# Performance work log

Hardware: AMD Instinct MI355X
Metric: run time of the kernel (lower is better)

The kernel has to match this reference:

```python
import jax, jax.numpy as jnp
import numpy as np

N, B, DIN = 128, 2, 128
D, DFF, NHEAD, NLAYERS = 256, 1024, 8, 2
BLOCK = 32
LENGTH = 160


def setup_inputs() -> dict:
    key = jax.random.key(0)
    ks = jax.random.split(key, 10)
    r = lambda k, sh: jax.random.normal(k, sh, jnp.float32) * 0.05
    return {
        "inputs": jax.random.normal(ks[0], (N, B, DIN), jnp.float32),
        "in_W1": r(ks[1], (DIN, DFF)), "in_b1": jnp.zeros((DFF,), jnp.float32),
        "in_W2": r(ks[2], (DFF, D)), "in_b2": jnp.zeros((D,), jnp.float32),
        "k_W1": r(ks[3], (DIN, DFF)), "k_b1": jnp.zeros((DFF,), jnp.float32),
        "k_W2": r(ks[4], (DFF, 2)), "k_b2": jnp.zeros((2,), jnp.float32),
        "Wqkv": r(ks[5], (NLAYERS, D, 3 * D)), "bqkv": jnp.zeros((NLAYERS, 3 * D), jnp.float32),
        "Wo": r(ks[6], (NLAYERS, D, D)), "bo": jnp.zeros((NLAYERS, D), jnp.float32),
        "ln1_g": jnp.ones((NLAYERS, D), jnp.float32), "ln1_b": jnp.zeros((NLAYERS, D), jnp.float32),
        "W1": r(ks[7], (NLAYERS, D, DFF)), "b1": jnp.zeros((NLAYERS, DFF), jnp.float32),
        "W2": r(ks[8], (NLAYERS, DFF, D)), "b2": jnp.zeros((NLAYERS, D), jnp.float32),
        "ln2_g": jnp.ones((NLAYERS, D), jnp.float32), "ln2_b": jnp.zeros((NLAYERS, D), jnp.float32),
        "length": LENGTH,
    }


def _ln(x, g, b):
    m = jnp.mean(x, axis=-1, keepdims=True)
    v = jnp.mean(jnp.square(x - m), axis=-1, keepdims=True)
    return (x - m) * jax.lax.rsqrt(v + 1e-5) * g + b


def _forward(inputs, in_W1, in_b1, in_W2, in_b2, k_W1, k_b1, k_W2, k_b2,
             Wqkv, bqkv, Wo, bo, ln1_g, ln1_b, W1, b1, W2, b2, ln2_g, ln2_b, length):
    n, b, din = inputs.shape
    d = in_W2.shape[1]
    H, dh = NHEAD, in_W2.shape[1] // NHEAD
    Wmax = 2 * BLOCK + 1
    L = length
    idx = jnp.arange(n)
    starts = jnp.maximum(0, idx - BLOCK)                 # [N]
    ends = jnp.minimum(L, idx + BLOCK + 1)               # [N]
    cols = starts[:, None] + jnp.arange(Wmax)[None, :]   # [N,Wmax] absolute column per window slot
    valid = cols < ends[:, None]                          # [N,Wmax] ragged-window mask

    # sinusoidal PE at absolute column positions (start_idx = max(0, i-block))
    pos = cols.astype(jnp.float32)
    div = jnp.exp(jnp.arange(0, din, 2, dtype=jnp.float32) * (-np.log(10000.0) / din))
    ang = pos[..., None] * div                            # [N,Wmax,din/2]
    pe = jnp.stack([jnp.sin(ang), jnp.cos(ang)], axis=-1).reshape(n, Wmax, din)

    # row token repeated across its window + PE, then input_ff
    x = inputs[:, None, :, :] + pe[:, :, None, :]         # [N,Wmax,B,din]
    h = jnp.maximum(x @ in_W1 + in_b1, 0.0) @ in_W2 + in_b2  # [N,Wmax,B,D]

    # TransformerEncoder (post-norm, relu, eval mode) over the window axis, padded slots masked as keys
    kmask = valid[:, None, None, None, :]                 # [N,1,1,1,Wmax]
    scale = 1.0 / np.sqrt(dh)
    for l in range(Wqkv.shape[0]):
        qkv = h @ Wqkv[l] + bqkv[l]
        q, k, v = [t.reshape(n, Wmax, b, H, dh) for t in jnp.split(qkv, 3, axis=-1)]
        s = jnp.einsum('nqbhe,nkbhe->nbhqk', q, k) * scale
        s = jnp.where(kmask, s, -jnp.inf)
        a = jax.nn.softmax(s, axis=-1)
        o = jnp.einsum('nbhqk,nkbhe->nqbhe', a, v).reshape(n, Wmax, b, d)
        h = _ln(h + o @ Wo[l] + bo[l], ln1_g[l], ln1_b[l])
        f = jnp.maximum(h @ W1[l] + b1[l], 0.0) @ W2[l] + b2[l]
        h = _ln(h + f, ln2_g[l], ln2_b[l])

    # hierarchy kernel scores (Gaussian band kernel with learned (mu, logsig) per row/batch)
    kp = jnp.maximum(inputs @ k_W1 + k_b1, 0.0) @ k_W2 + k_b2   # [N,B,2]
    hscale = L / n
    diff = cols.astype(jnp.float32) - idx[:, None].astype(jnp.float32) * hscale  # [N,Wmax]
    hier = -jnp.square(diff[:, :, None] - kp[:, None, :, 0]) * jnp.exp(kp[:, None, :, 1])  # [N,Wmax,B]

    # scatter banded values/scores into dense [N,L,...] then row-softmax and weighted combine
    n_idx = jnp.broadcast_to(idx[:, None], (n, Wmax))
    scat = jnp.where(valid, cols, L)                      # out-of-bounds -> dropped
    v_mat = jnp.zeros((n, L, b, d), jnp.float32).at[n_idx, scat].set(h, mode='drop')
    h_mat = jnp.full((n, L, b), -jnp.inf, jnp.float32).at[n_idx, scat].set(hier, mode='drop')
    w = jax.nn.softmax(h_mat, axis=0)[..., None]          # softmax over rows per column
    return jnp.sum(v_mat * w, axis=0)                     # [L,B,D]


def reference(inputs, in_W1, in_b1, in_W2, in_b2, k_W1, k_b1, k_W2, k_b2,
              Wqkv, bqkv, Wo, bo, ln1_g, ln1_b, W1, b1, W2, b2, ln2_g, ln2_b, length):
    return _forward(inputs, in_W1, in_b1, in_W2, in_b2, k_W1, k_b1, k_W2, k_b2,
                    Wqkv, bqkv, Wo, bo, ln1_g, ln1_b, W1, b1, W2, b2, ln2_g, ln2_b, length)
```

## Files before the change

kernel.cpp:

```cpp
#include <hip/hip_runtime.h>

constexpr int NN    = 128;
constexpr int BB    = 2;
constexpr int DIN   = 128;
constexpr int DD    = 256;
constexpr int DFF   = 1024;
constexpr int NH    = 8;
constexpr int DH    = 32;
constexpr int NL    = 2;
constexpr int BLK   = 32;
constexpr int WMAX  = 2 * BLK + 1;
constexpr int RROWS = NN * WMAX * BB;

typedef __attribute__((ext_vector_type(8))) short s16x8;
typedef __attribute__((ext_vector_type(4))) float f32x4;

__device__ __forceinline__ ushort f2bf(float f) {
  unsigned u = __float_as_uint(f);
  unsigned r = (u + 0x7fffu + ((u >> 16) & 1u)) >> 16;
  return (ushort)r;
}
__device__ __forceinline__ float bf2f(ushort h) {
  return __uint_as_float(((unsigned)h) << 16);
}

__device__ __forceinline__ void gld16(const void* g, void* l) {
  __builtin_amdgcn_global_load_lds(
      (const __attribute__((address_space(1))) void*)g,
      (__attribute__((address_space(3))) void*)l, 16, 0, 0);
}
__device__ __forceinline__ void vmdrain() {
  asm volatile("s_waitcnt vmcnt(0)" ::: "memory");
}

struct TD { const float* in; ushort* out; int K; int N; };
struct TPack { TD d[10]; };
constexpr int KP_BLOCKS   = NN * BB;
constexpr int WCONV_TILES = 1920;

__global__ __launch_bounds__(256) void k_prep(
    TPack p, const float* __restrict__ inp,
    const float* __restrict__ kW1, const float* __restrict__ kb1,
    const float* __restrict__ kW2, const float* __restrict__ kb2,
    float* __restrict__ kp) {
  __shared__ float ls[32 * 33];
  int bid = blockIdx.x;
  int tid = threadIdx.x;
  if (bid < KP_BLOCKS) {
    int row = bid;
    float* xs = ls;
    float* red = ls + 256;
    if (tid < DIN) xs[tid] = inp[row * DIN + tid];
    __syncthreads();
    int j0 = tid * 4;
    float4 acc = *(const float4*)(kb1 + j0);
#pragma unroll 8
    for (int k = 0; k < DIN; ++k) {
      float xv = xs[k];
      float4 wv = *(const float4*)(kW1 + (size_t)k * DFF + j0);
      acc.x += xv * wv.x; acc.y += xv * wv.y;
      acc.z += xv * wv.z; acc.w += xv * wv.w;
    }
    acc.x = fmaxf(acc.x, 0.f); acc.y = fmaxf(acc.y, 0.f);
    acc.z = fmaxf(acc.z, 0.f); acc.w = fmaxf(acc.w, 0.f);
    float4 w2a = *(const float4*)(kW2 + 2 * j0);
    float4 w2b = *(const float4*)(kW2 + 2 * j0 + 4);
    float a0 = acc.x * w2a.x + acc.y * w2a.z + acc.z * w2b.x + acc.w * w2b.z;
    float a1 = acc.x * w2a.y + acc.y * w2a.w + acc.z * w2b.y + acc.w * w2b.w;
#pragma unroll
    for (int m = 32; m > 0; m >>= 1) {
      a0 += __shfl_xor(a0, m, 64);
      a1 += __shfl_xor(a1, m, 64);
    }
    if ((tid & 63) == 0) { red[(tid >> 6) * 2] = a0; red[(tid >> 6) * 2 + 1] = a1; }
    __syncthreads();
    if (tid == 0) {
      kp[row * 2 + 0] = red[0] + red[2] + red[4] + red[6] + kb2[0];
      kp[row * 2 + 1] = red[1] + red[3] + red[5] + red[7] + kb2[1];
    }
  } else {
    const int cum[11] = {0, 128, 384, 576, 768, 832, 896, 1152, 1408, 1664, 1920};
    int tb = bid - KP_BLOCKS;
    int mi = 0;
#pragma unroll
    for (int i = 0; i < 10; ++i) if (tb >= cum[i + 1]) mi = i + 1;
    TD t = p.d[mi];
    int tile = tb - cum[mi];
    int ntk = t.K >> 5;
    int tn = tile / ntk, tk = tile - tn * ntk;
    int r = tid >> 5, c = tid & 31;
#pragma unroll
    for (int i = 0; i < 4; ++i) {
      int kk = r + 8 * i;
      ls[kk * 33 + c] = t.in[(size_t)(tk * 32 + kk) * t.N + tn * 32 + c];
    }
    __syncthreads();
#pragma unroll
    for (int i = 0; i < 4; ++i) {
      int rr = r + 8 * i;
      t.out[(size_t)(tn * 32 + rr) * t.K + tk * 32 + c] = f2bf(ls[c * 33 + rr]);
    }
  }
}

__global__ __launch_bounds__(512) void k_inmlp1(
    const float* __restrict__ inp, const ushort* __restrict__ Bt,
    const float* __restrict__ bias, ushort* __restrict__ out) {
  __shared__ __align__(16) char As[128 * 128];
  __shared__ __align__(16) char Bs[256 * 128];
  int tid = threadIdx.x;
  int m0 = blockIdx.x * 128, n0 = blockIdx.y * 256;
  int lane = tid & 63, w = tid >> 6;
  int wr = w >> 2, wc = w & 3;
  int fr = lane & 15, g = lane >> 4;
  f32x4 acc[4][4] = {};

  for (int kb = 0; kb < DIN; kb += 64) {
    for (int e = tid; e < 256 * 8; e += 512) {
      int row = e >> 3, c = e & 7;
      gld16(Bt + (size_t)(n0 + row) * DIN + kb + ((c ^ (row & 7)) * 8), Bs + e * 16);
    }
    for (int e = tid; e < 128 * 8; e += 512) {
      int row = e >> 3, c = e & 7;
      int r = m0 + row;
      int n = r / (WMAX * BB);
      int rem = r - n * (WMAX * BB);
      int wn = rem >> 1, b = rem & 1;
      int st = n - BLK; if (st < 0) st = 0;
      float pos = (float)(st + wn);
      const float* ip = inp + (n * BB + b) * DIN + kb + c * 8;
      ushort vals[8];
#pragma unroll
      for (int u = 0; u < 8; ++u) {
        int i = kb + c * 8 + u;
        float div = __expf(-0.0719557841f * (float)(i & 126));
        float ang = pos * div;
        float pe = (i & 1) ? __cosf(ang) : __sinf(ang);
        vals[u] = f2bf(ip[u] + pe);
      }
      *(uint4*)(As + ((row * 128 + c * 16) ^ ((row & 7) << 4))) = *(const uint4*)vals;
    }
    vmdrain();
    __syncthreads();
#pragma unroll
    for (int ks = 0; ks < 2; ++ks) {
      int kByte = ks * 64 + g * 16;
      s16x8 a[4], b[4];
#pragma unroll
      for (int m = 0; m < 4; ++m) {
        int row = wr * 64 + m * 16 + fr;
        a[m] = *(const s16x8*)(As + ((row * 128 + kByte) ^ ((row & 7) << 4)));
      }
#pragma unroll
      for (int n = 0; n < 4; ++n) {
        int row = wc * 64 + n * 16 + fr;
        b[n] = *(const s16x8*)(Bs + ((row * 128 + kByte) ^ ((row & 7) << 4)));
      }
#pragma unroll
      for (int m = 0; m < 4; ++m)
#pragma unroll
        for (int n = 0; n < 4; ++n)
          acc[m][n] = __builtin_amdgcn_mfma_f32_16x16x32_bf16(a[m], b[n], acc[m][n], 0, 0, 0);
    }
    __syncthreads();
  }
#pragma unroll
  for (int m = 0; m < 4; ++m) {
    int rowb = m0 + wr * 64 + m * 16 + g * 4;
#pragma unroll
    for (int n = 0; n < 4; ++n) {
      int col = n0 + wc * 64 + n * 16 + fr;
      float bv = bias[col];
#pragma unroll
      for (int j = 0; j < 4; ++j)
        out[(size_t)(rowb + j) * DFF + col] = f2bf(fmaxf(acc[m][n][j] + bv, 0.f));
    }
  }
}

template<int BMT, int RELU, int FUSE_LN, int BK>
__global__ __launch_bounds__(512) void k_gemm8(
    const ushort* __restrict__ A, const ushort* __restrict__ Bt,
    const float* __restrict__ bias, const ushort* __restrict__ resid,
    const float* __restrict__ lng, const float* __restrict__ lnb,
    ushort* __restrict__ out, int N, int K) {
  constexpr int MF   = BMT / 32;
  constexpr int CPR  = BK / 8;
  constexpr int ROWB = BK * 2;
  __shared__ __align__(16) char As[BMT * ROWB];
  __shared__ __align__(16) char Bs[256 * ROWB];
  int tid = threadIdx.x;
  int m0 = blockIdx.x * BMT, n0 = blockIdx.y * 256;
  int lane = tid & 63, w = tid >> 6;
  int wr = w >> 2, wc = w & 3;
  int fr = lane & 15, g = lane >> 4;
  f32x4 acc[MF][4] = {};

  for (int kb = 0; kb < K; kb += BK) {
    for (int e = tid; e < BMT * CPR; e += 512) {
      int row = e / CPR, c = e % CPR;
      gld16(A + (size_t)(m0 + row) * K + kb + ((c ^ (row & 7)) * 8), As + e * 16);
    }
    for (int e = tid; e < 256 * CPR; e += 512) {
      int row = e / CPR, c = e % CPR;
      gld16(Bt + (size_t)(n0 + row) * K + kb + ((c ^ (row & 7)) * 8), Bs + e * 16);
    }
    vmdrain();
    __syncthreads();
#pragma unroll
    for (int ks = 0; ks < BK / 32; ++ks) {
      int kByte = ks * 64 + g * 16;
      s16x8 a[MF], b[4];
#pragma unroll
      for (int m = 0; m < MF; ++m) {
        int row = wr * (BMT / 2) + m * 16 + fr;
        a[m] = *(const s16x8*)(As + ((row * ROWB + kByte) ^ ((row & 7) << 4)));
      }
#pragma unroll
      for (int n = 0; n < 4; ++n) {
        int row = wc * 64 + n * 16 + fr;
        b[n] = *(const s16x8*)(Bs + ((row * ROWB + kByte) ^ ((row & 7) << 4)));
      }
#pragma unroll
      for (int m = 0; m < MF; ++m)
#pragma unroll
        for (int n = 0; n < 4; ++n)
          acc[m][n] = __builtin_amdgcn_mfma_f32_16x16x32_bf16(a[m], b[n], acc[m][n], 0, 0, 0);
    }
    __syncthreads();
  }

  if constexpr (!FUSE_LN) {
#pragma unroll
    for (int m = 0; m < MF; ++m) {
      int rowb = m0 + wr * (BMT / 2) + m * 16 + g * 4;
#pragma unroll
      for (int n = 0; n < 4; ++n) {
        int col = n0 + wc * 64 + n * 16 + fr;
        float bv = bias[col];
#pragma unroll
        for (int j = 0; j < 4; ++j) {
          float v = acc[m][n][j] + bv;
          if (RELU) v = fmaxf(v, 0.f);
          out[(size_t)(rowb + j) * N + col] = f2bf(v);
        }
      }
    }
  } else {
    float* psum = (float*)As;
    float* psq  = (float*)(As + 4 * BMT * 4);
#pragma unroll
    for (int m = 0; m < MF; ++m) {
      int rowb = wr * (BMT / 2) + m * 16 + g * 4;
#pragma unroll
      for (int j = 0; j < 4; ++j) {
        float ps = 0.f, pq = 0.f;
#pragma unroll
        for (int n = 0; n < 4; ++n) {
          int col = wc * 64 + n * 16 + fr;
          float v = acc[m][n][j] + bias[col]
                  + bf2f(resid[(size_t)(m0 + rowb + j) * 256 + col]);
          acc[m][n][j] = v;
          ps += v; pq += v * v;
        }
#pragma unroll
        for (int d = 1; d < 16; d <<= 1) {
          ps += __shfl_xor(ps, d, 64);
          pq += __shfl_xor(pq, d, 64);
        }
        if (fr == 0) { psum[wc * BMT + rowb + j] = ps; psq[wc * BMT + rowb + j] = pq; }
      }
    }
    __syncthreads();
#pragma unroll
    for (int m = 0; m < MF; ++m) {
      int rowb = wr * (BMT / 2) + m * 16 + g * 4;
#pragma unroll
      for (int j = 0; j < 4; ++j) {
        int lr = rowb + j;
        float sm = psum[lr] + psum[BMT + lr] + psum[2 * BMT + lr] + psum[3 * BMT + lr];
        float sq = psq[lr] + psq[BMT + lr] + psq[2 * BMT + lr] + psq[3 * BMT + lr];
        float mean = sm * (1.f / 256.f);
        float var = sq * (1.f / 256.f) - mean * mean;
        float rs = rsqrtf(var + 1e-5f);
#pragma unroll
        for (int n = 0; n < 4; ++n) {
          int col = wc * 64 + n * 16 + fr;
          float v = (acc[m][n][j] - mean) * rs * lng[col] + lnb[col];
          out[(size_t)(m0 + lr) * 256 + col] = f2bf(v);
        }
      }
    }
  }
}

constexpr int QKS = 40;
constexpr int VTS = 104;
constexpr int PS  = 104;

__device__ __forceinline__ int vslot(int d, int r) {
  int rc = r >> 3;
  int sw = (rc < 8) ? (rc ^ (d >> 3)) : rc;
  return d * VTS + sw * 8 + (r & 7);
}

__global__ __launch_bounds__(320) void k_attn(
    const ushort* __restrict__ qkv, ushort* __restrict__ o,
    const int* __restrict__ lenp) {
  __shared__ __align__(16) ushort Ks[80 * QKS];
  __shared__ __align__(16) ushort Vt[32 * VTS];
  __shared__ __align__(16) ushort Pb[5 * 16 * PS];
  int L = lenp[0];
  int blk = blockIdx.x;
  int hh = blk >> 8;
  int nb = blk & 255;
  int b = nb & 1;
  int n = nb >> 1;
  int s0 = n - BLK; if (s0 < 0) s0 = 0;
  int e0 = n + BLK + 1; if (e0 > L) e0 = L;
  int vn = e0 - s0;
  int tid = threadIdx.x;

  for (int i = tid; i < 32 * VTS / 2; i += 320) ((uint*)Vt)[i] = 0;
  for (int i = tid; i < 15 * QKS / 2; i += 320)
    ((uint*)(Ks + 65 * QKS))[i] = 0;
  __syncthreads();
  for (int e = tid; e < 65 * 4; e += 320) {
    int r = e >> 2, c = e & 3;
    const ushort* base = qkv + ((size_t)(n * WMAX + r) * BB + b) * (3 * DD) + hh * DH;
    *(uint4*)(Ks + r * QKS + c * 8) = *(const uint4*)(base + DD + c * 8);
    uint4 vv = *(const uint4*)(base + 2 * DD + c * 8);
    const ushort* vp = (const ushort*)&vv;
#pragma unroll
    for (int u = 0; u < 8; ++u) Vt[vslot(c * 8 + u, r)] = vp[u];
  }

  int w = tid >> 6, lane = tid & 63;
  int fr = lane & 15, g = lane >> 4;
  int q0 = w * 16;
  ushort* Pw = Pb + w * 16 * PS;

  int qr_ld = q0 + fr; if (qr_ld > 64) qr_ld = 64;
  s16x8 aq = *(const s16x8*)(qkv + ((size_t)(n * WMAX + qr_ld) * BB + b) * (3 * DD)
                             + hh * DH + g * 8);
  __syncthreads();

  f32x4 sacc[5];
#pragma unroll
  for (int t = 0; t < 5; ++t) {
    s16x8 bk = *(const s16x8*)(Ks + (t * 16 + fr) * QKS + g * 8);
    f32x4 z = {0.f, 0.f, 0.f, 0.f};
    sacc[t] = __builtin_amdgcn_mfma_f32_16x16x32_bf16(aq, bk, z, 0, 0, 0);
  }
  const float scl = 0.17677669529663687f;
#pragma unroll
  for (int j = 0; j < 4; ++j) {
    float pv[5];
    float mx = -3e38f;
#pragma unroll
    for (int t = 0; t < 5; ++t) {
      bool ok = (t * 16 + fr) < vn;
      pv[t] = ok ? sacc[t][j] * scl : -3e38f;
      mx = fmaxf(mx, pv[t]);
    }
#pragma unroll
    for (int d = 1; d < 16; d <<= 1) mx = fmaxf(mx, __shfl_xor(mx, d, 64));
    float sum = 0.f;
#pragma unroll
    for (int t = 0; t < 5; ++t) {
      float e = ((t * 16 + fr) < vn) ? __expf(pv[t] - mx) : 0.f;
      pv[t] = e;
      sum += e;
    }
#pragma unroll
    for (int d = 1; d < 16; d <<= 1) sum += __shfl_xor(sum, d, 64);
    float inv = 1.f / sum;
#pragma unroll
    for (int t = 0; t < 5; ++t)
      Pw[(g * 4 + j) * PS + t * 16 + fr] = f2bf(pv[t] * inv);
  }
  {
    int zr = lane >> 2, zc = 80 + (lane & 3) * 4;
    *(uint2*)(Pw + zr * PS + zc) = make_uint2(0u, 0u);
  }
  __syncthreads();

  f32x4 oacc[2] = {};
#pragma unroll
  for (int k0 = 0; k0 < 3; ++k0) {
    s16x8 ap = *(const s16x8*)(Pw + fr * PS + k0 * 32 + g * 8);
#pragma unroll
    for (int nt = 0; nt < 2; ++nt) {
      s16x8 bv = *(const s16x8*)(Vt + vslot(nt * 16 + fr, k0 * 32 + g * 8));
      oacc[nt] = __builtin_amdgcn_mfma_f32_16x16x32_bf16(ap, bv, oacc[nt], 0, 0, 0);
    }
  }
#pragma unroll
  for (int nt = 0; nt < 2; ++nt) {
#pragma unroll
    for (int j = 0; j < 4; ++j) {
      int qr = q0 + g * 4 + j;
      if (qr < WMAX)
        o[((size_t)(n * WMAX + qr) * BB + b) * DD + hh * DH + nt * 16 + fr] =
            f2bf(oacc[nt][j]);
    }
  }
}

__global__ __launch_bounds__(256) void k_final(
    const ushort* __restrict__ h, const float* __restrict__ kp,
    float* __restrict__ out, const int* __restrict__ lenp) {
  int L = lenp[0];
  int t = blockIdx.x >> 1, b = blockIdx.x & 1;
  float hsc = (float)L / (float)NN;
  int nlo = t - BLK; if (nlo < 0) nlo = 0;
  int nhi = t + BLK; if (nhi > NN - 1) nhi = NN - 1;
  float mx = -3e38f;
  for (int n = nlo; n <= nhi; ++n) {
    float kp0 = kp[(n * BB + b) * 2 + 0];
    float kp1 = kp[(n * BB + b) * 2 + 1];
    float dif = (float)t - (float)n * hsc - kp0;
    float lg = -dif * dif * __expf(kp1);
    mx = fmaxf(mx, lg);
  }
  float sum = 0.f, acc = 0.f;
  int c = threadIdx.x;
  for (int n = nlo; n <= nhi; ++n) {
    float kp0 = kp[(n * BB + b) * 2 + 0];
    float kp1 = kp[(n * BB + b) * 2 + 1];
    float dif = (float)t - (float)n * hsc - kp0;
    float lg = -dif * dif * __expf(kp1);
    float p = __expf(lg - mx);
    sum += p;
    int st = n - BLK; if (st < 0) st = 0;
    int w = t - st;
    acc += p * bf2f(h[(size_t)((n * WMAX + w) * BB + b) * DD + c]);
  }
  out[(size_t)(t * BB + b) * DD + c] = acc / sum;
}

extern "C" void kernel_launch(void* const* d_in, const int* in_sizes, int n_in,
                              void* d_out, int out_size, void* d_ws, size_t ws_size,
                              hipStream_t stream) {
  const float* inputs = (const float*)d_in[0];
  const float* in_W1  = (const float*)d_in[1];
  const float* in_b1  = (const float*)d_in[2];
  const float* in_W2  = (const float*)d_in[3];
  const float* in_b2  = (const float*)d_in[4];
  const float* k_W1   = (const float*)d_in[5];
  const float* k_b1   = (const float*)d_in[6];
  const float* k_W2   = (const float*)d_in[7];
  const float* k_b2   = (const float*)d_in[8];
  const float* Wqkv   = (const float*)d_in[9];
  const float* bqkv   = (const float*)d_in[10];
  const float* Wo     = (const float*)d_in[11];
  const float* bo     = (const float*)d_in[12];
  const float* ln1_g  = (const float*)d_in[13];
  const float* ln1_b  = (const float*)d_in[14];
  const float* W1     = (const float*)d_in[15];
  const float* b1     = (const float*)d_in[16];
  const float* W2     = (const float*)d_in[17];
  const float* b2     = (const float*)d_in[18];
  const float* ln2_g  = (const float*)d_in[19];
  const float* ln2_b  = (const float*)d_in[20];
  const int*   lenp   = (const int*)d_in[21];
  float* out = (float*)d_out;
  (void)in_sizes; (void)n_in; (void)ws_size;

  ushort* wsu = (ushort*)d_ws;
  size_t off = 0;
  auto alloc = [&](size_t nelem) { ushort* p = wsu + off; off += (nelem + 7) & ~7ull; return p; };
  ushort* inW1t = alloc((size_t)DFF * DIN);
  ushort* inW2t = alloc((size_t)DD * DFF);
  ushort* Wqkvt = alloc((size_t)NL * 3 * DD * DD);
  ushort* Wot   = alloc((size_t)NL * DD * DD);
  ushort* W1t   = alloc((size_t)NL * DFF * DD);
  ushort* W2t   = alloc((size_t)NL * DD * DFF);
  ushort* tq    = alloc((size_t)RROWS * DFF);
  ushort* hb    = alloc((size_t)RROWS * DD);
  ushort* ob    = alloc((size_t)RROWS * DD);
  float*  kp    = (float*)(wsu + off);

  int L = out_size / (BB * DD);

  TPack tp;
  tp.d[0] = {in_W1, inW1t, DIN, DFF};
  tp.d[1] = {in_W2, inW2t, DFF, DD};
  tp.d[2] = {Wqkv,                        Wqkvt,                       DD, 3 * DD};
  tp.d[3] = {Wqkv + (size_t)DD * 3 * DD,  Wqkvt + (size_t)3 * DD * DD, DD, 3 * DD};
  tp.d[4] = {Wo,                    Wot,                   DD, DD};
  tp.d[5] = {Wo + (size_t)DD * DD,  Wot + (size_t)DD * DD, DD, DD};
  tp.d[6] = {W1,                      W1t,                    DD, DFF};
  tp.d[7] = {W1 + (size_t)DD * DFF,   W1t + (size_t)DFF * DD, DD, DFF};
  tp.d[8] = {W2,                      W2t,                    DFF, DD};
  tp.d[9] = {W2 + (size_t)DFF * DD,   W2t + (size_t)DD * DFF, DFF, DD};

  k_prep<<<KP_BLOCKS + WCONV_TILES, 256, 0, stream>>>(
      tp, inputs, k_W1, k_b1, k_W2, k_b2, kp);

  k_inmlp1<<<dim3(RROWS / 128, 4), 512, 0, stream>>>(inputs, inW1t, in_b1, tq);
  k_gemm8<64, 0, 0, 128><<<dim3(RROWS / 64, 1), 512, 0, stream>>>(
      tq, inW2t, in_b2, nullptr, nullptr, nullptr, hb, DD, DFF);

  for (int l = 0; l < NL; ++l) {
    k_gemm8<128, 0, 0, 64><<<dim3(RROWS / 128, 3), 512, 0, stream>>>(
        hb, Wqkvt + (size_t)l * 3 * DD * DD, bqkv + (size_t)l * 3 * DD,
        nullptr, nullptr, nullptr, tq, 3 * DD, DD);
    k_attn<<<NN * BB * NH, 320, 0, stream>>>(tq, ob, lenp);
    k_gemm8<64, 0, 1, 128><<<dim3(RROWS / 64, 1), 512, 0, stream>>>(
        ob, Wot + (size_t)l * DD * DD, bo + (size_t)l * DD, hb,
        ln1_g + (size_t)l * DD, ln1_b + (size_t)l * DD, hb, DD, DD);
    k_gemm8<128, 1, 0, 64><<<dim3(RROWS / 128, 4), 512, 0, stream>>>(
        hb, W1t + (size_t)l * DFF * DD, b1 + (size_t)l * DFF,
        nullptr, nullptr, nullptr, tq, DFF, DD);
    k_gemm8<64, 0, 1, 128><<<dim3(RROWS / 64, 1), 512, 0, stream>>>(
        tq, W2t + (size_t)l * DD * DFF, b2 + (size_t)l * DD, hb,
        ln2_g + (size_t)l * DD, ln2_b + (size_t)l * DD, hb, DD, DFF);
  }
  k_final<<<L * BB, 256, 0, stream>>>(hb, kp, out, lenp);
}
```

Before: 262.3 us.

## Add double-buffered pipelined GEMM for K=1024 down-projections

Introduces k_gemmp, a 64x256-tile bf16 MFMA GEMM that stages the next K-tile into a second LDS buffer with global-to-LDS loads while computing the current one, using vmcnt waits to overlap memory and math. It replaces the previous k_gemm8 for the input MLP second projection and the FFN W2 projection (K=1024), keeping the bias and residual+LayerNorm epilogues. The goal is to hide global load latency across the long K loop; it doubles LDS usage, which may reduce occupancy.

Result: no change. 261.7 us (-0.2%).

```diff
diff --git a/kernel.cpp b/kernel.cpp
--- a/kernel.cpp
+++ b/kernel.cpp
@@ -280,6 +280,141 @@
         int lr = rowb + j;
         float sm = psum[lr] + psum[BMT + lr] + psum[2 * BMT + lr] + psum[3 * BMT + lr];
         float sq = psq[lr] + psq[BMT + lr] + psq[2 * BMT + lr] + psq[3 * BMT + lr];
+        float mean = sm * (1.f / 256.f);
+        float var = sq * (1.f / 256.f) - mean * mean;
+        float rs = rsqrtf(var + 1e-5f);
+#pragma unroll
+        for (int n = 0; n < 4; ++n) {
+          int col = wc * 64 + n * 16 + fr;
+          float v = (acc[m][n][j] - mean) * rs * lng[col] + lnb[col];
+          out[(size_t)(m0 + lr) * 256 + col] = f2bf(v);
+        }
+      }
+    }
+  }
+}
+
+template<int RELU, int FUSE_LN>
+__global__ __launch_bounds__(512) void k_gemmp(
+    const ushort* __restrict__ A, const ushort* __restrict__ Bt,
+    const float* __restrict__ bias, const ushort* __restrict__ resid,
+    const float* __restrict__ lng, const float* __restrict__ lnb,
+    ushort* __restrict__ out, int N, int K) {
+  constexpr int BMT = 64;
+  __shared__ __align__(16) char As[2 * 64 * 128];
+  __shared__ __align__(16) char Bs[2 * 256 * 128];
+  int tid = threadIdx.x;
+  int m0 = blockIdx.x * BMT, n0 = blockIdx.y * 256;
+  int lane = tid & 63, w = tid >> 6;
+  int wr = w >> 2, wc = w & 3;
+  int fr = lane & 15, g = lane >> 4;
+  f32x4 acc[2][4] = {};
+
+  auto stage = [&](int half, int tk) {
+    int kb = tk * 64;
+    char* Ah = As + half * (64 * 128);
+    char* Bh = Bs + half * (256 * 128);
+    {
+      int e = tid;
+      int row = e >> 3, c = e & 7;
+      gld16(A + (size_t)(m0 + row) * K + kb + ((c ^ (row & 7)) * 8), Ah + e * 16);
+    }
+#pragma unroll
+    for (int it = 0; it < 4; ++it) {
+      int e = tid + it * 512;
+      int row = e >> 3, c = e & 7;
+      gld16(Bt + (size_t)(n0 + row) * K + kb + ((c ^ (row & 7)) * 8), Bh + e * 16);
+    }
+  };
+  auto compute = [&](int half) {
+    const char* Ah = As + half * (64 * 128);
+    const char* Bh = Bs + half * (256 * 128);
+#pragma unroll
+    for (int ks = 0; ks < 2; ++ks) {
+      int kByte = ks * 64 + g * 16;
+      s16x8 a[2], b[4];
+#pragma unroll
+      for (int m = 0; m < 2; ++m) {
+        int row = wr * 32 + m * 16 + fr;
+        a[m] = *(const s16x8*)(Ah + ((row * 128 + kByte) ^ ((row & 7) << 4)));
+      }
+#pragma unroll
+      for (int n = 0; n < 4; ++n) {
+        int row = wc * 64 + n * 16 + fr;
+        b[n] = *(const s16x8*)(Bh + ((row * 128 + kByte) ^ ((row & 7) << 4)));
+      }
+#pragma unroll
+      for (int m = 0; m < 2; ++m)
+#pragma unroll
+        for (int n = 0; n < 4; ++n)
+          acc[m][n] = __builtin_amdgcn_mfma_f32_16x16x32_bf16(a[m], b[n], acc[m][n], 0, 0, 0);
+    }
+  };
+
+  int nt = K >> 6;
+  stage(0, 0);
+  for (int t = 0; t < nt; ++t) {
+    if (t + 1 < nt) {
+      stage((t + 1) & 1, t + 1);
+      asm volatile("s_waitcnt vmcnt(5)" ::: "memory");
+    } else {
+      asm volatile("s_waitcnt vmcnt(0)" ::: "memory");
+    }
+    __syncthreads();
+    compute(t & 1);
+    __syncthreads();
+  }
+
+  if constexpr (!FUSE_LN) {
+#pragma unroll
+    for (int m = 0; m < 2; ++m) {
+      int rowb = m0 + wr * 32 + m * 16 + g * 4;
+#pragma unroll
+      for (int n = 0; n < 4; ++n) {
+        int col = n0 + wc * 64 + n * 16 + fr;
+        float bv = bias[col];
+#pragma unroll
+        for (int j = 0; j < 4; ++j) {
+          float v = acc[m][n][j] + bv;
+          if (RELU) v = fmaxf(v, 0.f);
+          out[(size_t)(rowb + j) * N + col] = f2bf(v);
+        }
+      }
+    }
+  } else {
+    float* psum = (float*)As;
+    float* psq  = (float*)(As + 4 * 64 * 4);
+#pragma unroll
+    for (int m = 0; m < 2; ++m) {
+      int rowb = wr * 32 + m * 16 + g * 4;
+#pragma unroll
+      for (int j = 0; j < 4; ++j) {
+        float ps = 0.f, pq = 0.f;
+#pragma unroll
+        for (int n = 0; n < 4; ++n) {
+          int col = wc * 64 + n * 16 + fr;
+          float v = acc[m][n][j] + bias[col]
+                  + bf2f(resid[(size_t)(m0 + rowb + j) * 256 + col]);
+          acc[m][n][j] = v;
+          ps += v; pq += v * v;
+        }
+#pragma unroll
+        for (int d = 1; d < 16; d <<= 1) {
+          ps += __shfl_xor(ps, d, 64);
+          pq += __shfl_xor(pq, d, 64);
+        }
+        if (fr == 0) { psum[wc * 64 + rowb + j] = ps; psq[wc * 64 + rowb + j] = pq; }
+      }
+    }
+    __syncthreads();
+#pragma unroll
+    for (int m = 0; m < 2; ++m) {
+      int rowb = wr * 32 + m * 16 + g * 4;
+#pragma unroll
+      for (int j = 0; j < 4; ++j) {
+        int lr = rowb + j;
+        float sm = psum[lr] + psum[64 + lr] + psum[128 + lr] + psum[192 + lr];
+        float sq = psq[lr] + psq[64 + lr] + psq[128 + lr] + psq[192 + lr];
         float mean = sm * (1.f / 256.f);
         float var = sq * (1.f / 256.f) - mean * mean;
         float rs = rsqrtf(var + 1e-5f);
@@ -499,7 +634,7 @@
       tp, inputs, k_W1, k_b1, k_W2, k_b2, kp);
 
   k_inmlp1<<<dim3(RROWS / 128, 4), 512, 0, stream>>>(inputs, inW1t, in_b1, tq);
-  k_gemm8<64, 0, 0, 128><<<dim3(RROWS / 64, 1), 512, 0, stream>>>(
+  k_gemmp<0, 0><<<dim3(RROWS / 64, 1), 512, 0, stream>>>(
       tq, inW2t, in_b2, nullptr, nullptr, nullptr, hb, DD, DFF);
 
   for (int l = 0; l < NL; ++l) {
@@ -513,7 +648,7 @@
     k_gemm8<128, 1, 0, 64><<<dim3(RROWS / 128, 4), 512, 0, stream>>>(
         hb, W1t + (size_t)l * DFF * DD, b1 + (size_t)l * DFF,
         nullptr, nullptr, nullptr, tq, DFF, DD);
-    k_gemm8<64, 0, 1, 128><<<dim3(RROWS / 64, 1), 512, 0, stream>>>(
+    k_gemmp<0, 1><<<dim3(RROWS / 64, 1), 512, 0, stream>>>(
         tq, W2t + (size_t)l * DD * DFF, b2 + (size_t)l * DD, hb,
         ln2_g + (size_t)l * DD, ln2_b + (size_t)l * DD, hb, DD, DFF);
   }
```
